# Kernel optimization log

Hardware: AMD Instinct MI355X
Metric: run time of the kernel (lower is better)

Reference implementation:

```python
import jax, jax.numpy as jnp
import numpy as np

N = 10000      # nodes
E = 160000     # edges
MUL = 16       # multiplicity of 0e and 1o irreps
NB = 16        # num radial basis
H = 64         # radial MLP hidden
WN = 4 * MUL * MUL  # tensor-product weight_numel (4 CG paths, uvw weights)


def setup_inputs() -> dict:
    key = jax.random.key(0)
    ks = jax.random.split(key, 10)
    node_features = jax.random.normal(ks[0], (N, 4 * MUL), dtype=jnp.float32)  # [N, 16 + 16*3]
    edge_index = jax.random.randint(ks[1], (2, E), 0, N)
    edge_sh = jax.random.normal(ks[2], (E, 4), dtype=jnp.float32)              # 1x0e + 1x1o
    edge_radial_emb = jax.random.uniform(ks[3], (E, NB), dtype=jnp.float32)
    # RadialMLP params
    w1 = jax.random.normal(ks[4], (NB, H), dtype=jnp.float32) / np.sqrt(NB).astype(np.float32)
    b1 = jnp.zeros((H,), jnp.float32)
    w2 = jax.random.normal(ks[5], (H, WN), dtype=jnp.float32) / np.sqrt(H).astype(np.float32)
    b2 = jnp.zeros((WN,), jnp.float32)
    # equivariant Linear params (one [mul,mul] mix per irrep)
    lin_w0 = jax.random.normal(ks[6], (MUL, MUL), dtype=jnp.float32)
    lin_w1 = jax.random.normal(ks[7], (MUL, MUL), dtype=jnp.float32)
    return dict(node_features=node_features, edge_sh=edge_sh, edge_radial_emb=edge_radial_emb,
                w1=w1, b1=b1, w2=w2, b2=b2, lin_w0=lin_w0, lin_w1=lin_w1,
                edge_index=edge_index)


def reference(node_features, edge_sh, edge_radial_emb, w1, b1, w2, b2, lin_w0, lin_w1, edge_index):
    n = node_features.shape[0]
    src, dst = edge_index[0], edge_index[1]
    # radial MLP -> per-edge tensor-product weights, split into the 4 CG paths
    tpw = jax.nn.silu(edge_radial_emb @ w1 + b1) @ w2 + b2        # [E, 4*MUL*MUL]
    W = tpw.reshape(-1, 4, MUL, MUL)
    W00, W01, W10, W11 = W[:, 0], W[:, 1], W[:, 2], W[:, 3]
    # gather source node features, split into scalar (0e) and vector (1o) parts
    xf = node_features[src]
    xs = xf[:, :MUL]                                              # [E, MUL]
    xv = xf[:, MUL:].reshape(-1, MUL, 3)                          # [E, MUL, 3]
    shs = edge_sh[:, 0:1]                                         # [E, 1]
    shv = edge_sh[:, 1:4]                                         # [E, 3]
    alpha = np.float32(1.0 / np.sqrt(2.0 * MUL))  # path norm: 2 paths feed each output irrep
    inv_sqrt3 = np.float32(1.0 / np.sqrt(3.0))    # w3j(1,1,0) contraction constant
    # scalar messages: 0e*0e->0e and 1o*1o->0e
    msg_s = alpha * (jnp.einsum('eu,euv->ev', xs * shs, W00)
                     + inv_sqrt3 * jnp.einsum('eui,ei,euv->ev', xv, shv, W11))
    # vector messages: 0e*1o->1o and 1o*0e->1o
    msg_v = alpha * (jnp.einsum('eu,euv,ei->evi', xs, W01, shv)
                     + jnp.einsum('eui,euv->evi', xv * shs[:, :, None], W10))
    # scatter-sum messages into destination nodes
    agg_s = jax.ops.segment_sum(msg_s, dst, num_segments=n)       # [N, MUL]
    agg_v = jax.ops.segment_sum(msg_v, dst, num_segments=n)       # [N, MUL, 3]
    # equivariant linear (channel mixing per irrep, 1/sqrt(fan_in) norm)
    s = np.float32(1.0 / np.sqrt(MUL))
    ts = (agg_s @ lin_w0) * s
    tv = jnp.einsum('nui,uv->nvi', agg_v, lin_w1) * s
    # NormActivation: x * silu(||x||)/||x||
    eps = np.float32(1e-8)
    ns = jnp.abs(ts)
    act_s = ts * (jax.nn.silu(ns) / (ns + eps))
    nv = jnp.sqrt(jnp.sum(tv * tv, axis=-1))
    act_v = tv * (jax.nn.silu(nv) / (nv + eps))[..., None]
    # identity skip (input irreps == output irreps)
    return node_features + jnp.concatenate([act_s, act_v.reshape(n, MUL * 3)], axis=-1)
```

## Files before the change

### kernel.cpp

```cpp
#include <hip/hip_runtime.h>
#include <hip/hip_bf16.h>
#include <math.h>

#define EPB 64
#define ALPHA 0.17677669529663687f
#define INV_SQRT3 0.57735026918962576f

typedef __attribute__((ext_vector_type(8))) short short8;
typedef __attribute__((ext_vector_type(4))) float f32x4;

__device__ __forceinline__ float silu_f(float x) { return x / (1.0f + __expf(-x)); }

__device__ __forceinline__ unsigned short bf16_rne(float x) {
  unsigned int u = __float_as_uint(x);
  unsigned int r = u + 0x7fffu + ((u >> 16) & 1u);
  return (unsigned short)(r >> 16);
}

__device__ __forceinline__ void ld4bf(float* d, const unsigned short* s) {
  const uint2 t = *(const uint2*)s;
  d[0] = __uint_as_float(t.x << 16);
  d[1] = __uint_as_float(t.x & 0xffff0000u);
  d[2] = __uint_as_float(t.y << 16);
  d[3] = __uint_as_float(t.y & 0xffff0000u);
}

__global__ __launch_bounds__(256) void prep_kernel(const float* __restrict__ w2,
                                                   unsigned short* __restrict__ w2t,
                                                   const int* __restrict__ eidx,
                                                   int* __restrict__ deg,
                                                   int* __restrict__ rank, int E) {
  if (blockIdx.x < 16) {
    __shared__ unsigned short tile[16][260];
    const int t = threadIdx.x;
    const int k0 = (blockIdx.x & 3) * 16;
    const int c0 = (blockIdx.x >> 2) * 256;
    #pragma unroll
    for (int j = 0; j < 16; ++j)
      tile[j][t] = bf16_rne(w2[(size_t)(k0 + j) * 1024 + c0 + t]);
    __syncthreads();
    union { unsigned short s[16]; uint4 q[2]; } pk;
    #pragma unroll
    for (int j = 0; j < 16; ++j) pk.s[j] = tile[j][t];
    uint4* dst = (uint4*)&w2t[(size_t)(c0 + t) * 64 + k0];
    dst[0] = pk.q[0];
    dst[1] = pk.q[1];
  } else {
    const int e = (blockIdx.x - 16) * 256 + threadIdx.x;
    if (e < E) rank[e] = atomicAdd(&deg[eidx[E + e]], 1);
  }
}

__global__ __launch_bounds__(256) void scan_kernel(const int* __restrict__ deg,
                                                   int* __restrict__ offs, int N) {
  __shared__ int sums[256];
  const int t = threadIdx.x;
  const int ch = (N + 255) >> 8;
  const int lo = t * ch;
  const int hi = min(lo + ch, N);
  int s = 0;
  for (int i = lo; i < hi; ++i) s += deg[i];
  sums[t] = s;
  __syncthreads();
  #pragma unroll
  for (int d = 1; d < 256; d <<= 1) {
    int v = (t >= d) ? sums[t - d] : 0;
    __syncthreads();
    sums[t] += v;
    __syncthreads();
  }
  int run = sums[t] - s;
  for (int i = lo; i < hi; ++i) { offs[i] = run; run += deg[i]; }
  if (lo < N && hi == N) offs[N] = run;
}

__global__ __launch_bounds__(256, 3) void tfn_edge_kernel(
    const float* __restrict__ nf,
    const float* __restrict__ esh,
    const float* __restrict__ emb,
    const float* __restrict__ w1g,
    const float* __restrict__ b1g,
    const unsigned short* __restrict__ w2t,
    const float* __restrict__ b2g,
    const int*   __restrict__ eidx,
    const int*   __restrict__ rank,
    const int*   __restrict__ offs,
    float* __restrict__ msg,
    float* __restrict__ agg,
    int E, int posmode)
{
  __shared__ __align__(16) unsigned short hsm[EPB * 72];
  __shared__ __align__(16) float t01[2 * 1088];
  __shared__ __align__(16) float t2s[1088];
  __shared__ __align__(16) float t3s[3 * 1088];
  __shared__ __align__(16) unsigned short fsT[16 * 72];
  __shared__ __align__(16) unsigned short fbT[16 * 72];
  __shared__ __align__(16) unsigned short fxvT[48 * 72];
  __shared__ __align__(16) float b2s[1024];
  __shared__ float shs_l[EPB];
  __shared__ float shv_l[EPB * 3];
  __shared__ int   pos_l[EPB];

  const int tid = threadIdx.x;
  const int ebase = blockIdx.x * EPB;

  float* embs = t01;
  float* w1s  = t01 + 1088;

  {
    const int e = tid >> 2, p = tid & 3;
    int eg = ebase + e; if (eg >= E) eg = E - 1;

    const float4 em = *(const float4*)&emb[(size_t)eg * 16 + p * 4];
    embs[e * 17 + p * 4 + 0] = em.x;
    embs[e * 17 + p * 4 + 1] = em.y;
    embs[e * 17 + p * 4 + 2] = em.z;
    embs[e * 17 + p * 4 + 3] = em.w;

    const float4 sh = *(const float4*)&esh[(size_t)eg * 4];
    if (p == 0) {
      shs_l[e] = sh.x;
      shv_l[e * 3 + 0] = sh.y; shv_l[e * 3 + 1] = sh.z; shv_l[e * 3 + 2] = sh.w;
      const int dst = eidx[E + eg];
      pos_l[e] = posmode ? (offs[dst] + rank[eg]) : dst;
    }

    const int src = eidx[eg];
    const float4* row4 = (const float4*)(nf + (size_t)src * 64);
    const float4 xs4 = row4[p];
    const float4 va  = row4[4 + p * 3 + 0];
    const float4 vb  = row4[4 + p * 3 + 1];
    const float4 vc  = row4[4 + p * 3 + 2];
    const float xsr[4] = {xs4.x, xs4.y, xs4.z, xs4.w};
    const float xvf[12] = {va.x, va.y, va.z, va.w, vb.x, vb.y, vb.z, vb.w,
                           vc.x, vc.y, vc.z, vc.w};
    #pragma unroll
    for (int uu = 0; uu < 4; ++uu) {
      const int u = p * 4 + uu;
      const float x0 = xvf[uu * 3 + 0];
      const float x1 = xvf[uu * 3 + 1];
      const float x2 = xvf[uu * 3 + 2];
      fsT[u * 72 + e] = bf16_rne(xsr[uu]);
      fbT[u * 72 + e] = bf16_rne(x0 * sh.y + x1 * sh.z + x2 * sh.w);
      fxvT[(0 * 16 + u) * 72 + e] = bf16_rne(x0);
      fxvT[(1 * 16 + u) * 72 + e] = bf16_rne(x1);
      fxvT[(2 * 16 + u) * 72 + e] = bf16_rne(x2);
    }
  }
  {
    const int r = tid >> 4, c4 = (tid & 15) * 4;
    *(float4*)&w1s[r * 64 + c4] = *(const float4*)&w1g[r * 64 + c4];
  }
  *(float4*)&b2s[tid * 4] = *(const float4*)&b2g[tid * 4];
  __syncthreads();

  {
    const int e = tid >> 2, p = tid & 3;
    #pragma unroll
    for (int kk = 0; kk < 16; ++kk) {
      const int c = p * 16 + kk;
      float acc = b1g[c];
      #pragma unroll
      for (int j = 0; j < 16; ++j) acc = fmaf(embs[e * 17 + j], w1s[j * 64 + c], acc);
      hsm[e * 72 + c] = bf16_rne(silu_f(acc));
    }
  }
  __syncthreads();

  const int lane = tid & 63;
  const int sec  = tid >> 6;
  const int q = lane >> 4, m = lane & 15;

  union AF { uint4 u4; short8 s8; };
  AF afr[4][2];
  #pragma unroll
  for (int mt = 0; mt < 4; ++mt)
    #pragma unroll
    for (int ks = 0; ks < 2; ++ks)
      afr[mt][ks].u4 = *(const uint4*)&hsm[(mt * 16 + m) * 72 + ks * 32 + q * 8];

  const unsigned short* ftab = (sec == 3) ? fbT : fsT;
  const uint4* w2tq = (const uint4*)w2t;
  const uint4* bp = w2tq + ((size_t)(sec * 256 + m)) * 8 + q;

  float accA[4][4] = {};
  float accB[4][4] = {};
  float accC[4][4] = {};

  AF b0v, b1v;
  b0v.u4 = bp[0];
  b1v.u4 = bp[4];

  #pragma unroll 2
  for (int u = 0; u < 16; ++u) {
    AF n0, n1;
    if (u < 15) {
      n0.u4 = bp[(u + 1) * 128];
      n1.u4 = bp[(u + 1) * 128 + 4];
    }
    const float b2v = b2s[sec * 256 + u * 16 + m];

    #pragma unroll
    for (int mt = 0; mt < 4; ++mt) {
      f32x4 c = {0.0f, 0.0f, 0.0f, 0.0f};
      c = __builtin_amdgcn_mfma_f32_16x16x32_bf16(afr[mt][0].s8, b0v.s8, c, 0, 0, 0);
      c = __builtin_amdgcn_mfma_f32_16x16x32_bf16(afr[mt][1].s8, b1v.s8, c, 0, 0, 0);

      const int fo = mt * 16 + q * 4;
      float fA[4], fB[4], fC[4];
      if (sec == 2) {
        ld4bf(fA, &fxvT[(0 * 16 + u) * 72 + fo]);
        ld4bf(fB, &fxvT[(1 * 16 + u) * 72 + fo]);
        ld4bf(fC, &fxvT[(2 * 16 + u) * 72 + fo]);
        #pragma unroll
        for (int r = 0; r < 4; ++r) {
          const float tp = c[r] + b2v;
          accA[mt][r] = fmaf(fA[r], tp, accA[mt][r]);
          accB[mt][r] = fmaf(fB[r], tp, accB[mt][r]);
          accC[mt][r] = fmaf(fC[r], tp, accC[mt][r]);
        }
      } else {
        ld4bf(fA, &ftab[u * 72 + fo]);
        #pragma unroll
        for (int r = 0; r < 4; ++r)
          accA[mt][r] = fmaf(fA[r], c[r] + b2v, accA[mt][r]);
      }
    }
    b0v = n0;
    b1v = n1;
  }

  #pragma unroll
  for (int mt = 0; mt < 4; ++mt)
    #pragma unroll
    for (int r = 0; r < 4; ++r) {
      const int e = mt * 16 + q * 4 + r;
      if (sec == 0)      t01[e * 17 + m]        = accA[mt][r] * shs_l[e];
      else if (sec == 1) t2s[e * 17 + m]        = accA[mt][r];
      else if (sec == 3) t01[1088 + e * 17 + m] = accA[mt][r];
      else {
        const float s = shs_l[e];
        t3s[0 * 1088 + e * 17 + m] = accA[mt][r] * s;
        t3s[1 * 1088 + e * 17 + m] = accB[mt][r] * s;
        t3s[2 * 1088 + e * 17 + m] = accC[mt][r] * s;
      }
    }
  __syncthreads();

  {
    const int w = tid >> 6, lc = tid & 63;
    const int cc = lc - 16;
    const int v  = cc / 3;
    const int i3 = cc - v * 3;
    #pragma unroll 1
    for (int t8 = 0; t8 < 16; ++t8) {
      const int e = w * 16 + t8;
      if (ebase + e < E) {
        float val;
        if (lc < 16) {
          val = ALPHA * (t01[e * 17 + lc] + INV_SQRT3 * t01[1088 + e * 17 + lc]);
        } else {
          val = ALPHA * (t2s[e * 17 + v] * shv_l[e * 3 + i3] + t3s[i3 * 1088 + e * 17 + v]);
        }
        if (posmode) msg[(size_t)pos_l[e] * 64 + lc] = val;
        else         atomicAdd(&agg[(size_t)pos_l[e] * 64 + lc], val);
      }
    }
  }
}

__global__ __launch_bounds__(256) void tfn_agg_node_kernel(
    const float* __restrict__ msg, const int* __restrict__ offs,
    const float* __restrict__ nf, const float* __restrict__ lw0,
    const float* __restrict__ lw1, float* __restrict__ out, int N)
{
  __shared__ float ag[4 * 68];
  __shared__ float w0s[256], w1s[256];
  const int t = threadIdx.x;
  w0s[t] = lw0[t];
  w1s[t] = lw1[t];

  const int n0 = blockIdx.x * 4;
  {
    const int w = t >> 6, lane = t & 63;
    const int n = n0 + w;
    if (n < N) {
      const int s = offs[n], e = offs[n + 1];
      float a0 = 0.0f, a1 = 0.0f, a2 = 0.0f, a3 = 0.0f;
      int j = s;
      for (; j + 3 < e; j += 4) {
        a0 += msg[(size_t)(j + 0) * 64 + lane];
        a1 += msg[(size_t)(j + 1) * 64 + lane];
        a2 += msg[(size_t)(j + 2) * 64 + lane];
        a3 += msg[(size_t)(j + 3) * 64 + lane];
      }
      for (; j < e; ++j) a0 += msg[(size_t)j * 64 + lane];
      ag[w * 68 + lane] = (a0 + a1) + (a2 + a3);
    }
  }
  __syncthreads();
  {
    const int node = t >> 6, c = t & 63;
    const int n = n0 + node;
    if (n >= N) return;
    const float* a = &ag[node * 68];
    float val;
    if (c < 16) {
      float accv = 0.0f;
      #pragma unroll
      for (int u = 0; u < 16; ++u) accv = fmaf(a[u], w0s[u * 16 + c], accv);
      const float ts = 0.25f * accv;
      const float ns = fabsf(ts);
      const float g = (ns / (1.0f + __expf(-ns))) / (ns + 1e-8f);
      val = ts * g;
    } else {
      const int cc = c - 16;
      const int v = cc / 3, i = cc - v * 3;
      float a0 = 0.0f, a1 = 0.0f, a2 = 0.0f;
      #pragma unroll
      for (int u = 0; u < 16; ++u) {
        const float w = w1s[u * 16 + v];
        a0 = fmaf(a[16 + u * 3 + 0], w, a0);
        a1 = fmaf(a[16 + u * 3 + 1], w, a1);
        a2 = fmaf(a[16 + u * 3 + 2], w, a2);
      }
      a0 *= 0.25f; a1 *= 0.25f; a2 *= 0.25f;
      const float nv = sqrtf(a0 * a0 + a1 * a1 + a2 * a2);
      const float g = (nv / (1.0f + __expf(-nv))) / (nv + 1e-8f);
      val = ((i == 0) ? a0 : (i == 1) ? a1 : a2) * g;
    }
    out[(size_t)n * 64 + c] = nf[(size_t)n * 64 + c] + val;
  }
}

__global__ __launch_bounds__(256) void tfn_node_kernel(
    const float* __restrict__ nf,
    const float* __restrict__ lw0,
    const float* __restrict__ lw1,
    float* __restrict__ out, int N)
{
  __shared__ float w0s[256], w1s[256];
  const int tid = threadIdx.x;
  w0s[tid] = lw0[tid];
  w1s[tid] = lw1[tid];
  __syncthreads();

  const int n = blockIdx.x * 256 + tid;
  if (n >= N) return;

  float* rowp = out + (size_t)n * 64;
  float as[16], av[16][3];
  #pragma unroll
  for (int u = 0; u < 16; ++u) as[u] = rowp[u];
  #pragma unroll
  for (int u = 0; u < 16; ++u) {
    av[u][0] = rowp[16 + u * 3 + 0];
    av[u][1] = rowp[16 + u * 3 + 1];
    av[u][2] = rowp[16 + u * 3 + 2];
  }
  const float* nfr = nf + (size_t)n * 64;
  float res[64];

  #pragma unroll
  for (int v = 0; v < 16; ++v) {
    float acc = 0.0f;
    #pragma unroll
    for (int u = 0; u < 16; ++u) acc = fmaf(as[u], w0s[u * 16 + v], acc);
    const float ts = 0.25f * acc;
    const float ns = fabsf(ts);
    const float g = (ns / (1.0f + __expf(-ns))) / (ns + 1e-8f);
    res[v] = nfr[v] + ts * g;
  }
  #pragma unroll
  for (int v = 0; v < 16; ++v) {
    float a0 = 0.0f, a1 = 0.0f, a2 = 0.0f;
    #pragma unroll
    for (int u = 0; u < 16; ++u) {
      const float w = w1s[u * 16 + v];
      a0 = fmaf(av[u][0], w, a0);
      a1 = fmaf(av[u][1], w, a1);
      a2 = fmaf(av[u][2], w, a2);
    }
    a0 *= 0.25f; a1 *= 0.25f; a2 *= 0.25f;
    const float nv = sqrtf(a0 * a0 + a1 * a1 + a2 * a2);
    const float g = (nv / (1.0f + __expf(-nv))) / (nv + 1e-8f);
    res[16 + v * 3 + 0] = nfr[16 + v * 3 + 0] + a0 * g;
    res[16 + v * 3 + 1] = nfr[16 + v * 3 + 1] + a1 * g;
    res[16 + v * 3 + 2] = nfr[16 + v * 3 + 2] + a2 * g;
  }
  #pragma unroll
  for (int o = 0; o < 64; o += 4) {
    *(float4*)&rowp[o] = make_float4(res[o], res[o + 1], res[o + 2], res[o + 3]);
  }
}

extern "C" void kernel_launch(void* const* d_in, const int* in_sizes, int n_in,
                              void* d_out, int out_size, void* d_ws, size_t ws_size,
                              hipStream_t stream) {
  const float* nf  = (const float*)d_in[0];
  const float* esh = (const float*)d_in[1];
  const float* emb = (const float*)d_in[2];
  const float* w1  = (const float*)d_in[3];
  const float* b1  = (const float*)d_in[4];
  const float* w2  = (const float*)d_in[5];
  const float* b2  = (const float*)d_in[6];
  const float* lw0 = (const float*)d_in[7];
  const float* lw1 = (const float*)d_in[8];
  const int*   eix = (const int*)d_in[9];

  const int N = in_sizes[0] / 64;
  const int E = in_sizes[9] / 2;
  float* out = (float*)d_out;

  char* ws = (char*)d_ws;
  const size_t o_w2t  = 0;
  const size_t o_deg  = 131072;
  const size_t o_offs = o_deg  + (((size_t)N * 4 + 15) & ~(size_t)15);
  const size_t o_rank = o_offs + (((size_t)(N + 1) * 4 + 15) & ~(size_t)15);
  const size_t o_msg  = (o_rank + (size_t)E * 4 + 255) & ~(size_t)255;
  const size_t need   = o_msg + (size_t)E * 256;
  const int posmode = (ws_size >= need) ? 1 : 0;

  unsigned short* w2t = (unsigned short*)(ws + o_w2t);
  int*   deg  = (int*)(ws + o_deg);
  int*   offs = (int*)(ws + o_offs);
  int*   rankp = (int*)(ws + o_rank);
  float* msg  = (float*)(ws + o_msg);

  const int eblocks = (E + EPB - 1) / EPB;

  if (posmode) {
    hipMemsetAsync(deg, 0, (size_t)N * 4, stream);
    prep_kernel<<<dim3(16 + (E + 255) / 256), dim3(256), 0, stream>>>(
        w2, w2t, eix, deg, rankp, E);
    scan_kernel<<<dim3(1), dim3(256), 0, stream>>>(deg, offs, N);
    tfn_edge_kernel<<<dim3(eblocks), dim3(256), 0, stream>>>(
        nf, esh, emb, w1, b1, w2t, b2, eix, rankp, offs, msg, out, E, 1);
    tfn_agg_node_kernel<<<dim3((N + 3) / 4), dim3(256), 0, stream>>>(
        msg, offs, nf, lw0, lw1, out, N);
  } else {
    prep_kernel<<<dim3(16), dim3(256), 0, stream>>>(w2, w2t, eix, nullptr, nullptr, 0);
    hipMemsetAsync(out, 0, (size_t)out_size * sizeof(float), stream);
    tfn_edge_kernel<<<dim3(eblocks), dim3(256), 0, stream>>>(
        nf, esh, emb, w1, b1, w2t, b2, eix, nullptr, nullptr, nullptr, out, E, 0);
    tfn_node_kernel<<<dim3((N + 255) / 256), dim3(256), 0, stream>>>(nf, lw0, lw1, out, N);
  }
}
```

Measured before the change: 188.9 us.

## Shrink edge-kernel LDS with bf16 staging, raise occupancy, widen scan

The edge kernel's per-edge intermediate tiles (t01, t2s, t3s) are now stored in shared memory as bf16 instead of fp32. All shared buffers are packed into one aliased byte array so the block's LDS footprint drops and launch bounds can request four blocks per CU instead of three. The b2 bias is folded into the MFMA accumulator init, and the single-block scan kernel now uses 1024 threads to shorten its serial per-thread loops. The cost is extra rounding of intermediate messages to bf16, plus more register pressure under the tighter occupancy target.

```diff
diff --git a/kernel.cpp b/kernel.cpp
--- a/kernel.cpp
+++ b/kernel.cpp
@@ -15,6 +15,10 @@
   unsigned int u = __float_as_uint(x);
   unsigned int r = u + 0x7fffu + ((u >> 16) & 1u);
   return (unsigned short)(r >> 16);
+}
+
+__device__ __forceinline__ float bf2f(unsigned short s) {
+  return __uint_as_float(((unsigned int)s) << 16);
 }
 
 __device__ __forceinline__ void ld4bf(float* d, const unsigned short* s) {
@@ -51,11 +55,11 @@
   }
 }
 
-__global__ __launch_bounds__(256) void scan_kernel(const int* __restrict__ deg,
-                                                   int* __restrict__ offs, int N) {
-  __shared__ int sums[256];
+__global__ __launch_bounds__(1024) void scan_kernel(const int* __restrict__ deg,
+                                                    int* __restrict__ offs, int N) {
+  __shared__ int sums[1024];
   const int t = threadIdx.x;
-  const int ch = (N + 255) >> 8;
+  const int ch = (N + 1023) >> 10;
   const int lo = t * ch;
   const int hi = min(lo + ch, N);
   int s = 0;
@@ -63,7 +67,7 @@
   sums[t] = s;
   __syncthreads();
   #pragma unroll
-  for (int d = 1; d < 256; d <<= 1) {
+  for (int d = 1; d < 1024; d <<= 1) {
     int v = (t >= d) ? sums[t - d] : 0;
     __syncthreads();
     sums[t] += v;
@@ -74,7 +78,7 @@
   if (lo < N && hi == N) offs[N] = run;
 }
 
-__global__ __launch_bounds__(256, 3) void tfn_edge_kernel(
+__global__ __launch_bounds__(256, 4) void tfn_edge_kernel(
     const float* __restrict__ nf,
     const float* __restrict__ esh,
     const float* __restrict__ emb,
@@ -89,23 +93,23 @@
     float* __restrict__ agg,
     int E, int posmode)
 {
-  __shared__ __align__(16) unsigned short hsm[EPB * 72];
-  __shared__ __align__(16) float t01[2 * 1088];
-  __shared__ __align__(16) float t2s[1088];
-  __shared__ __align__(16) float t3s[3 * 1088];
-  __shared__ __align__(16) unsigned short fsT[16 * 72];
-  __shared__ __align__(16) unsigned short fbT[16 * 72];
-  __shared__ __align__(16) unsigned short fxvT[48 * 72];
-  __shared__ __align__(16) float b2s[1024];
-  __shared__ float shs_l[EPB];
-  __shared__ float shv_l[EPB * 3];
-  __shared__ int   pos_l[EPB];
+  __shared__ __align__(16) unsigned char smem[39168];
+  unsigned short* t01  = (unsigned short*)(smem + 0);
+  unsigned short* t2s  = (unsigned short*)(smem + 4352);
+  unsigned short* t3s  = (unsigned short*)(smem + 6528);
+  unsigned short* hsm  = (unsigned short*)(smem + 13056);
+  unsigned short* fsT  = (unsigned short*)(smem + 22272);
+  unsigned short* fbT  = (unsigned short*)(smem + 24576);
+  unsigned short* fxvT = (unsigned short*)(smem + 26880);
+  float* b2s   = (float*)(smem + 33792);
+  float* shs_l = (float*)(smem + 37888);
+  float* shv_l = (float*)(smem + 38144);
+  int*   pos_l = (int*)(smem + 38912);
+  float* embs = (float*)(smem + 0);
+  float* w1s  = (float*)(smem + 4352);
 
   const int tid = threadIdx.x;
   const int ebase = blockIdx.x * EPB;
-
-  float* embs = t01;
-  float* w1s  = t01 + 1088;
 
   {
     const int e = tid >> 2, p = tid & 3;
@@ -202,7 +206,7 @@
 
     #pragma unroll
     for (int mt = 0; mt < 4; ++mt) {
-      f32x4 c = {0.0f, 0.0f, 0.0f, 0.0f};
+      f32x4 c = {b2v, b2v, b2v, b2v};
       c = __builtin_amdgcn_mfma_f32_16x16x32_bf16(afr[mt][0].s8, b0v.s8, c, 0, 0, 0);
       c = __builtin_amdgcn_mfma_f32_16x16x32_bf16(afr[mt][1].s8, b1v.s8, c, 0, 0, 0);
 
@@ -214,20 +218,18 @@
         ld4bf(fC, &fxvT[(2 * 16 + u) * 72 + fo]);
         #pragma unroll
         for (int r = 0; r < 4; ++r) {
-          const float tp = c[r] + b2v;
-          accA[mt][r] = fmaf(fA[r], tp, accA[mt][r]);
-          accB[mt][r] = fmaf(fB[r], tp, accB[mt][r]);
-          accC[mt][r] = fmaf(fC[r], tp, accC[mt][r]);
+          accA[mt][r] = fmaf(fA[r], c[r], accA[mt][r]);
+          accB[mt][r] = fmaf(fB[r], c[r], accB[mt][r]);
+          accC[mt][r] = fmaf(fC[r], c[r], accC[mt][r]);
         }
       } else {
         ld4bf(fA, &ftab[u * 72 + fo]);
         #pragma unroll
         for (int r = 0; r < 4; ++r)
-          accA[mt][r] = fmaf(fA[r], c[r] + b2v, accA[mt][r]);
+          accA[mt][r] = fmaf(fA[r], c[r], accA[mt][r]);
       }
     }
-    b0v = n0;
-    b1v = n1;
+    if (u < 15) { b0v = n0; b1v = n1; }
   }
 
   #pragma unroll
@@ -235,14 +237,14 @@
     #pragma unroll
     for (int r = 0; r < 4; ++r) {
       const int e = mt * 16 + q * 4 + r;
-      if (sec == 0)      t01[e * 17 + m]        = accA[mt][r] * shs_l[e];
-      else if (sec == 1) t2s[e * 17 + m]        = accA[mt][r];
-      else if (sec == 3) t01[1088 + e * 17 + m] = accA[mt][r];
+      if (sec == 0)      t01[e * 17 + m]        = bf16_rne(accA[mt][r] * shs_l[e]);
+      else if (sec == 1) t2s[e * 17 + m]        = bf16_rne(accA[mt][r]);
+      else if (sec == 3) t01[1088 + e * 17 + m] = bf16_rne(accA[mt][r]);
       else {
         const float s = shs_l[e];
-        t3s[0 * 1088 + e * 17 + m] = accA[mt][r] * s;
-        t3s[1 * 1088 + e * 17 + m] = accB[mt][r] * s;
-        t3s[2 * 1088 + e * 17 + m] = accC[mt][r] * s;
+        t3s[0 * 1088 + e * 17 + m] = bf16_rne(accA[mt][r] * s);
+        t3s[1 * 1088 + e * 17 + m] = bf16_rne(accB[mt][r] * s);
+        t3s[2 * 1088 + e * 17 + m] = bf16_rne(accC[mt][r] * s);
       }
     }
   __syncthreads();
@@ -258,9 +260,10 @@
       if (ebase + e < E) {
         float val;
         if (lc < 16) {
-          val = ALPHA * (t01[e * 17 + lc] + INV_SQRT3 * t01[1088 + e * 17 + lc]);
+          val = ALPHA * (bf2f(t01[e * 17 + lc]) + INV_SQRT3 * bf2f(t01[1088 + e * 17 + lc]));
         } else {
-          val = ALPHA * (t2s[e * 17 + v] * shv_l[e * 3 + i3] + t3s[i3 * 1088 + e * 17 + v]);
+          val = ALPHA * (bf2f(t2s[e * 17 + v]) * shv_l[e * 3 + i3] +
+                         bf2f(t3s[i3 * 1088 + e * 17 + v]));
         }
         if (posmode) msg[(size_t)pos_l[e] * 64 + lc] = val;
         else         atomicAdd(&agg[(size_t)pos_l[e] * 64 + lc], val);
@@ -433,7 +436,7 @@
     hipMemsetAsync(deg, 0, (size_t)N * 4, stream);
     prep_kernel<<<dim3(16 + (E + 255) / 256), dim3(256), 0, stream>>>(
         w2, w2t, eix, deg, rankp, E);
-    scan_kernel<<<dim3(1), dim3(256), 0, stream>>>(deg, offs, N);
+    scan_kernel<<<dim3(1), dim3(1024), 0, stream>>>(deg, offs, N);
     tfn_edge_kernel<<<dim3(eblocks), dim3(256), 0, stream>>>(
         nf, esh, emb, w1, b1, w2t, b2, eix, rankp, offs, msg, out, E, 1);
     tfn_agg_node_kernel<<<dim3((N + 3) / 4), dim3(256), 0, stream>>>(
```

Measured after the change: 191.4 us. Within noise of the previous version (+1.3%).
